# Kernel tuning notes

Hardware: AMD Instinct MI355X
Metric: run time of the kernel (lower is better)

## Reference

```python
import jax, jax.numpy as jnp
import numpy as np

HEADS = 16
DIM_HEAD = 64
LN_EPS = 1e-5
COS_EPS = 1e-8


def setup_inputs() -> dict:
    key = jax.random.key(0)
    ks = jax.random.split(key, 5)
    dim = 1024
    inner = HEADS * DIM_HEAD
    q = jax.random.normal(ks[0], (4, 1024, dim), dtype=jnp.float32)
    k = jax.random.normal(ks[1], (4, 2048, dim), dtype=jnp.float32)
    v = jax.random.normal(ks[2], (4, 2048, dim), dtype=jnp.float32)
    W_in = jax.random.normal(ks[3], (dim, inner), dtype=jnp.float32) * (1.0 / np.sqrt(dim))
    W_out = jax.random.normal(ks[4], (inner, dim), dtype=jnp.float32) * (1.0 / np.sqrt(inner))
    ln_gamma = jnp.ones((dim,), dtype=jnp.float32)
    ln_beta = jnp.zeros((dim,), dtype=jnp.float32)
    b_out = jnp.zeros((dim,), dtype=jnp.float32)
    return {"q": q, "k": k, "v": v, "ln_gamma": ln_gamma, "ln_beta": ln_beta,
            "W_in": W_in, "W_out": W_out, "b_out": b_out}


def _layernorm(x, gamma, beta):
    mu = jnp.mean(x, axis=-1, keepdims=True)
    var = jnp.mean(jnp.square(x - mu), axis=-1, keepdims=True)  # biased, as torch
    return (x - mu) * jax.lax.rsqrt(var + LN_EPS) * gamma + beta


def _project(t, gamma, beta, W_in):
    # LayerNorm -> Linear(no bias) -> split heads: b n (h d) -> b h n d
    x = _layernorm(t, gamma, beta) @ W_in
    b, n, _ = x.shape
    return x.reshape(b, n, HEADS, DIM_HEAD).transpose(0, 2, 1, 3)


def reference(q, k, v, ln_gamma, ln_beta, W_in, W_out, b_out):
    f_q = _project(q, ln_gamma, ln_beta, W_in)  # [b,h,n,d]
    f_k = _project(k, ln_gamma, ln_beta, W_in)  # [b,h,m,d]
    f_v = _project(v, ln_gamma, ln_beta, W_in)  # [b,h,m,d]
    dots = jnp.einsum('bhnd,bhmd->bhnm', f_q, f_k)
    qn = jnp.linalg.norm(f_q, axis=-1, keepdims=True)          # [b,h,n,1]
    kn = jnp.linalg.norm(f_k, axis=-1, keepdims=True)          # [b,h,m,1]
    attn = dots / (qn * kn.transpose(0, 1, 3, 2) + COS_EPS)    # [b,h,n,m]
    out = jnp.einsum('bhnm,bhmd->bhnd', attn, f_v)             # [b,h,n,d]
    b, h, n, d = out.shape
    out = out.transpose(0, 2, 1, 3).reshape(b, n, h * d)       # b n (h d)
    return out @ W_out + b_out
```

## Files before the change

kernel.cpp:

```cpp
#include <hip/hip_runtime.h>

constexpr int BATCH = 4;
constexpr int SEQQ  = 1024;
constexpr int SEQK  = 2048;
constexpr int DIM   = 1024;
constexpr int NH    = 16;
constexpr int DH    = 64;
constexpr int RQ    = BATCH * SEQQ;
constexpr int RK    = BATCH * SEQK;
constexpr int RTOT  = RQ + 2 * RK;
constexpr int BH    = BATCH * NH;
constexpr int NSLC  = 8;
constexpr float LN_EPS = 1e-5f;

typedef _Float16 f16;
typedef __attribute__((ext_vector_type(8))) _Float16 f16x8;
typedef __attribute__((ext_vector_type(4))) float f32x4;

__device__ __forceinline__ void async16(const void* g, void* l) {
  __builtin_amdgcn_global_load_lds(
      (const __attribute__((address_space(1))) void*)g,
      (__attribute__((address_space(3))) void*)l, 16, 0, 0);
}

__global__ void __launch_bounds__(256) ln_to_f16(
    const float* __restrict__ q, const float* __restrict__ k,
    const float* __restrict__ v, const float* __restrict__ gamma,
    const float* __restrict__ beta, f16* __restrict__ a_h) {
  const int row = blockIdx.x * 4 + (threadIdx.x >> 6);
  const int lane = threadIdx.x & 63;
  const float* src;
  if (row < RQ)            src = q + (size_t)row * DIM;
  else if (row < RQ + RK)  src = k + (size_t)(row - RQ) * DIM;
  else                     src = v + (size_t)(row - RQ - RK) * DIM;
  float4 x[4];
  float s = 0.f, s2 = 0.f;
#pragma unroll
  for (int c = 0; c < 4; c++) {
    x[c] = ((const float4*)src)[c * 64 + lane];
    s  += x[c].x + x[c].y + x[c].z + x[c].w;
    s2 += x[c].x * x[c].x + x[c].y * x[c].y + x[c].z * x[c].z + x[c].w * x[c].w;
  }
#pragma unroll
  for (int off = 1; off < 64; off <<= 1) {
    s  += __shfl_xor(s, off);
    s2 += __shfl_xor(s2, off);
  }
  const float mu = s / DIM;
  const float rs = rsqrtf(s2 / DIM - mu * mu + LN_EPS);
#pragma unroll
  for (int c = 0; c < 4; c++) {
    float4 g = ((const float4*)gamma)[c * 64 + lane];
    float4 b = ((const float4*)beta)[c * 64 + lane];
    union { f16 h[4]; uint2 u; } o;
    o.h[0] = (f16)((x[c].x - mu) * rs * g.x + b.x);
    o.h[1] = (f16)((x[c].y - mu) * rs * g.y + b.y);
    o.h[2] = (f16)((x[c].z - mu) * rs * g.z + b.z);
    o.h[3] = (f16)((x[c].w - mu) * rs * g.w + b.w);
    ((uint2*)(a_h + (size_t)row * DIM))[c * 64 + lane] = o.u;
  }
}

__global__ void __launch_bounds__(256) transpose_f16(
    const float* __restrict__ W0, const float* __restrict__ W1,
    f16* __restrict__ T0, f16* __restrict__ T1) {
  const float* W = blockIdx.z ? W1 : W0;
  f16* T = blockIdx.z ? T1 : T0;
  __shared__ float tile[32][33];
  int tx = threadIdx.x & 31, ty = threadIdx.x >> 5;
  int k0 = blockIdx.x * 32, n0 = blockIdx.y * 32;
#pragma unroll
  for (int i = 0; i < 4; i++)
    tile[ty + 8 * i][tx] = W[(size_t)(k0 + ty + 8 * i) * DIM + n0 + tx];
  __syncthreads();
#pragma unroll
  for (int i = 0; i < 4; i++)
    T[(size_t)(n0 + ty + 8 * i) * DIM + k0 + tx] = (f16)tile[tx][ty + 8 * i];
}

template <int MT, bool OUT_F16, bool NORMS, bool BIAS>
__global__ void __launch_bounds__(256) mfma_gemm(
    const f16* __restrict__ A, const f16* __restrict__ Bt,
    void* __restrict__ Cout, const float* __restrict__ bias,
    float* __restrict__ rq, float* __restrict__ rk) {
  constexpr int JT = (MT == 128) ? 4 : 2;
  __shared__ f16 As[2][MT * 32];
  __shared__ f16 Bs[2][128 * 32];
  const int t = threadIdx.x;
  const int wid = t >> 6;
  const int lane = t & 63;
  const int row0 = blockIdx.x * MT;
  const int col0 = blockIdx.y * 128;
  const int wm = (MT == 128) ? (wid >> 1) * 64 : 0;
  const int wn = (MT == 128) ? (wid & 1) * 64 : wid * 32;

  const int rB = 32 * wid + (lane >> 2);
  const int qB = ((lane & 3) - ((rB >> 1) & 3)) & 3;
  const f16* gB = Bt + (size_t)(col0 + rB) * DIM + qB * 8;
  f16* lB0 = Bs[0] + 32 * wid * 32;
  f16* lB1 = Bs[1] + 32 * wid * 32;
  const int rA = (MT == 128 ? 32 : 16) * wid + (lane >> 2);
  const int qA = ((lane & 3) - ((rA >> 1) & 3)) & 3;
  const f16* gA = A + (size_t)(row0 + rA) * DIM + qA * 8;
  f16* lA0 = As[0] + (MT == 128 ? 32 : 16) * wid * 32;
  f16* lA1 = As[1] + (MT == 128 ? 32 : 16) * wid * 32;

  f32x4 acc[4][JT];
#pragma unroll
  for (int i = 0; i < 4; i++)
#pragma unroll
    for (int j = 0; j < JT; j++) acc[i][j] = (f32x4){0.f, 0.f, 0.f, 0.f};

  const int mrow = lane & 15;
  const int kq_p = (((lane >> 4) + ((lane >> 1) & 3)) & 3) * 8;

  for (int kt = 0; kt < DIM / 64; ++kt) {
    if (kt) __syncthreads();
    const int ko = kt * 64;
    async16(gA + ko,      lA0);
    if (MT == 128) async16(gA + ko + 16 * DIM, lA0 + 512);
    async16(gB + ko,      lB0);
    async16(gB + ko + 16 * DIM, lB0 + 512);
    async16(gA + ko + 32, lA1);
    if (MT == 128) async16(gA + ko + 32 + 16 * DIM, lA1 + 512);
    async16(gB + ko + 32, lB1);
    async16(gB + ko + 32 + 16 * DIM, lB1 + 512);
    __syncthreads();

#pragma unroll
    for (int h = 0; h < 2; ++h) {
      f16x8 af[4], bf[JT];
#pragma unroll
      for (int i = 0; i < 4; i++)
        af[i] = *(const f16x8*)(As[h] + (wm + i * 16 + mrow) * 32 + kq_p);
#pragma unroll
      for (int j = 0; j < JT; j++)
        bf[j] = *(const f16x8*)(Bs[h] + (wn + j * 16 + mrow) * 32 + kq_p);
#pragma unroll
      for (int i = 0; i < 4; i++)
#pragma unroll
        for (int j = 0; j < JT; j++)
          acc[i][j] = __builtin_amdgcn_mfma_f32_16x16x32_f16(af[i], bf[j], acc[i][j], 0, 0, 0);
    }
  }

  const int ccol = lane & 15;
  const int crow = (lane >> 4) * 4;
  if (OUT_F16) {
    f16* C = (f16*)Cout;
#pragma unroll
    for (int j = 0; j < JT; j++) {
      const int col = col0 + wn + j * 16 + ccol;
#pragma unroll
      for (int i = 0; i < 4; i++) {
        f16* Cp = C + (size_t)(row0 + wm + i * 16 + crow) * DIM + col;
#pragma unroll
        for (int r = 0; r < 4; r++) Cp[(size_t)r * DIM] = (f16)acc[i][j][r];
      }
    }
  } else {
    float* C = (float*)Cout;
#pragma unroll
    for (int j = 0; j < JT; j++) {
      const int col = col0 + wn + j * 16 + ccol;
      float bv = BIAS ? bias[col] : 0.f;
#pragma unroll
      for (int i = 0; i < 4; i++) {
        float* Cp = C + (size_t)(row0 + wm + i * 16 + crow) * DIM + col;
#pragma unroll
        for (int r = 0; r < 4; r++) Cp[(size_t)r * DIM] = acc[i][j][r] + bv;
      }
    }
  }

  if (NORMS && MT == 128) {
    float sums[4][4];
#pragma unroll
    for (int i = 0; i < 4; i++)
#pragma unroll
      for (int r = 0; r < 4; r++) {
        float s = 0.f;
#pragma unroll
        for (int j = 0; j < JT; j++) s += acc[i][j][r] * acc[i][j][r];
        sums[i][r] = s;
      }
#pragma unroll
    for (int off = 1; off < 16; off <<= 1)
#pragma unroll
      for (int i = 0; i < 4; i++)
#pragma unroll
        for (int r = 0; r < 4; r++)
          sums[i][r] += __shfl_xor(sums[i][r], off);
    if ((lane & 15) == 0) {
      const int head = (col0 + wn) >> 6;
#pragma unroll
      for (int i = 0; i < 4; i++)
#pragma unroll
        for (int r = 0; r < 4; r++) {
          const int row = row0 + wm + i * 16 + crow + r;
          const float inv = rsqrtf(sums[i][r]);
          if (row < RQ)            rq[(size_t)row * NH + head] = inv;
          else if (row < RQ + RK)  rk[(size_t)(row - RQ) * NH + head] = inv;
        }
    }
  }
}

__global__ void __launch_bounds__(256) s_kernel(
    const f16* __restrict__ f, const float* __restrict__ rk,
    float* __restrict__ S4) {
  const int bh = blockIdx.x;
  const int b = bh >> 4, h = bh & 15;
  const int mbase = blockIdx.y * (SEQK / NSLC);
  const int t = threadIdx.x;
  __shared__ float ks[32][68];
  __shared__ float vs[32][68];
  const int lm   = t >> 3;
  const int lseg = (t & 7) * 8;
  const int d1 = (t & 15) * 4;
  const int d2 = (t >> 4) * 4;
  float acc[4][4] = {{0.f}};
  const f16* fk_base = f + ((size_t)RQ + (size_t)b * SEQK) * DIM + h * DH;
  const f16* fv_base = f + ((size_t)RQ + RK + (size_t)b * SEQK) * DIM + h * DH;

  int m = mbase + lm;
  f16x8 kv = *(const f16x8*)(fk_base + (size_t)m * DIM + lseg);
  f16x8 vv = *(const f16x8*)(fv_base + (size_t)m * DIM + lseg);
  float sc = rk[(size_t)(b * SEQK + m) * NH + h];

  constexpr int SUBS = SEQK / NSLC / 32;
  for (int sub = 0; sub < SUBS; ++sub) {
    __syncthreads();
#pragma unroll
    for (int e = 0; e < 8; e++) {
      ks[lm][lseg + e] = (float)kv[e] * sc;
      vs[lm][lseg + e] = (float)vv[e];
    }
    __syncthreads();
    if (sub + 1 < SUBS) {
      m = mbase + (sub + 1) * 32 + lm;
      kv = *(const f16x8*)(fk_base + (size_t)m * DIM + lseg);
      vv = *(const f16x8*)(fv_base + (size_t)m * DIM + lseg);
      sc = rk[(size_t)(b * SEQK + m) * NH + h];
    }
#pragma unroll
    for (int mm = 0; mm < 32; ++mm) {
      float4 kk = *(const float4*)&ks[mm][d1];
      float4 vv2 = *(const float4*)&vs[mm][d2];
      acc[0][0] = fmaf(kk.x, vv2.x, acc[0][0]);
      acc[0][1] = fmaf(kk.x, vv2.y, acc[0][1]);
      acc[0][2] = fmaf(kk.x, vv2.z, acc[0][2]);
      acc[0][3] = fmaf(kk.x, vv2.w, acc[0][3]);
      acc[1][0] = fmaf(kk.y, vv2.x, acc[1][0]);
      acc[1][1] = fmaf(kk.y, vv2.y, acc[1][1]);
      acc[1][2] = fmaf(kk.y, vv2.z, acc[1][2]);
      acc[1][3] = fmaf(kk.y, vv2.w, acc[1][3]);
      acc[2][0] = fmaf(kk.z, vv2.x, acc[2][0]);
      acc[2][1] = fmaf(kk.z, vv2.y, acc[2][1]);
      acc[2][2] = fmaf(kk.z, vv2.z, acc[2][2]);
      acc[2][3] = fmaf(kk.z, vv2.w, acc[2][3]);
      acc[3][0] = fmaf(kk.w, vv2.x, acc[3][0]);
      acc[3][1] = fmaf(kk.w, vv2.y, acc[3][1]);
      acc[3][2] = fmaf(kk.w, vv2.z, acc[3][2]);
      acc[3][3] = fmaf(kk.w, vv2.w, acc[3][3]);
    }
  }
  float* Sp = S4 + ((size_t)blockIdx.y * BH + bh) * DH * DH;
#pragma unroll
  for (int i = 0; i < 4; i++)
#pragma unroll
    for (int j = 0; j < 4; j++)
      Sp[(d1 + i) * DH + (d2 + j)] = acc[i][j];
}

__global__ void __launch_bounds__(256) outhead_kernel(
    const f16* __restrict__ f, const float* __restrict__ S4,
    const float* __restrict__ rq, f16* __restrict__ ao) {
  const int bh = blockIdx.x;
  const int b = bh >> 4, h = bh & 15;
  const int nbase = blockIdx.y * 64;
  const int t = threadIdx.x;
  __shared__ float Sl[64][68];
  __shared__ float Ql[64][68];
  {
    const int r = t >> 2;
    const int seg = (t & 3) * 16;
    const float* Sp = S4 + (size_t)bh * DH * DH + r * DH + seg;
    constexpr size_t STR = (size_t)BH * DH * DH;
#pragma unroll
    for (int c = 0; c < 4; c++) {
      float4 s = {0.f, 0.f, 0.f, 0.f};
#pragma unroll
      for (int p = 0; p < NSLC; p++) {
        float4 sp = ((const float4*)(Sp + p * STR))[c];
        s.x += sp.x; s.y += sp.y; s.z += sp.z; s.w += sp.w;
      }
      *(float4*)&Sl[r][seg + 4 * c] = s;
    }
    const f16* Qp = f + ((size_t)b * SEQQ + nbase + r) * DIM + h * DH + seg;
    f16x8 q0 = *(const f16x8*)Qp;
    f16x8 q1 = *(const f16x8*)(Qp + 8);
#pragma unroll
    for (int e = 0; e < 8; e++) {
      Ql[r][seg + e]     = (float)q0[e];
      Ql[r][seg + 8 + e] = (float)q1[e];
    }
  }
  __syncthreads();
  const int d2 = (t & 15) * 4;
  const int g  = t >> 4;
#pragma unroll
  for (int i = 0; i < 4; ++i) {
    const int n = i * 16 + g;
    float4 acc = {0.f, 0.f, 0.f, 0.f};
#pragma unroll 8
    for (int d1 = 0; d1 < 64; ++d1) {
      float qv = Ql[n][d1];
      float4 sv = *(const float4*)&Sl[d1][d2];
      acc.x = fmaf(qv, sv.x, acc.x);
      acc.y = fmaf(qv, sv.y, acc.y);
      acc.z = fmaf(qv, sv.z, acc.z);
      acc.w = fmaf(qv, sv.w, acc.w);
    }
    const float r = rq[((size_t)b * SEQQ + nbase + n) * NH + h];
    union { f16 h4[4]; uint2 u; } o;
    o.h4[0] = (f16)(acc.x * r);
    o.h4[1] = (f16)(acc.y * r);
    o.h4[2] = (f16)(acc.z * r);
    o.h4[3] = (f16)(acc.w * r);
    *(uint2*)(ao + ((size_t)b * SEQQ + nbase + n) * DIM + h * DH + d2) = o.u;
  }
}

extern "C" void kernel_launch(void* const* d_in, const int* in_sizes, int n_in,
                              void* d_out, int out_size, void* d_ws, size_t ws_size,
                              hipStream_t stream) {
  const float* q     = (const float*)d_in[0];
  const float* k     = (const float*)d_in[1];
  const float* v     = (const float*)d_in[2];
  const float* gamma = (const float*)d_in[3];
  const float* beta  = (const float*)d_in[4];
  const float* W_in  = (const float*)d_in[5];
  const float* W_out = (const float*)d_in[6];
  const float* b_out = (const float*)d_in[7];
  float* out = (float*)d_out;

  char* w = (char*)d_ws;
  f16*   f      = (f16*)w;
  f16*   a_h    = f + (size_t)RTOT * DIM;
  f16*   wt_in  = a_h + (size_t)RTOT * DIM;
  f16*   wt_out = wt_in + (size_t)DIM * DIM;
  float* rqb    = (float*)(wt_out + (size_t)DIM * DIM);
  float* rkb    = rqb + (size_t)RQ * NH;
  float* S4     = rkb + (size_t)RK * NH;
  f16*   ao     = a_h;

  ln_to_f16<<<RTOT / 4, 256, 0, stream>>>(q, k, v, gamma, beta, a_h);
  transpose_f16<<<dim3(DIM / 32, DIM / 32, 2), 256, 0, stream>>>(
      W_in, W_out, wt_in, wt_out);

  mfma_gemm<128, true, true, false><<<dim3(RTOT / 128, DIM / 128), 256, 0, stream>>>(
      a_h, wt_in, f, nullptr, rqb, rkb);

  s_kernel<<<dim3(BH, NSLC), 256, 0, stream>>>(f, rkb, S4);

  outhead_kernel<<<dim3(BH, SEQQ / 64), 256, 0, stream>>>(f, S4, rqb, ao);

  mfma_gemm<64, false, false, true><<<dim3(RQ / 64, DIM / 128), 256, 0, stream>>>(
      ao, wt_out, out, b_out, nullptr, nullptr);
}
```

Before: 244.5 us.

## Fold per-head attention state into per-batch output weight matrix

Row normalisation now happens in the projection GEMM epilogue: each head segment is scaled by its inverse norm before the f16 store, so s_kernel no longer applies key scales. The per-head KᵀV matrices are reduced to f16 and multiplied into W_out to build a per-batch 1024x1024 matrix. The final GEMM then consumes normalized q directly against that matrix, replacing the separate outhead kernel. This trades the q·S pass and ao round-trip for an extra small GEMM, per-batch weight reads, and more f16 rounding of S and M.

```diff
diff --git a/kernel.cpp b/kernel.cpp
--- a/kernel.cpp
+++ b/kernel.cpp
@@ -78,11 +78,10 @@
     T[(size_t)(n0 + ty + 8 * i) * DIM + k0 + tx] = (f16)tile[tx][ty + 8 * i];
 }
 
-template <int MT, bool OUT_F16, bool NORMS, bool BIAS>
+template <int MT, bool OUT_F16, bool NORMS, bool BIAS, bool PERB>
 __global__ void __launch_bounds__(256) mfma_gemm(
     const f16* __restrict__ A, const f16* __restrict__ Bt,
-    void* __restrict__ Cout, const float* __restrict__ bias,
-    float* __restrict__ rq, float* __restrict__ rk) {
+    void* __restrict__ Cout, const float* __restrict__ bias) {
   constexpr int JT = (MT == 128) ? 4 : 2;
   __shared__ f16 As[2][MT * 32];
   __shared__ f16 Bs[2][128 * 32];
@@ -94,9 +93,11 @@
   const int wm = (MT == 128) ? (wid >> 1) * 64 : 0;
   const int wn = (MT == 128) ? (wid & 1) * 64 : wid * 32;
 
+  const f16* BtB = PERB ? Bt + (size_t)(row0 >> 10) * DIM * DIM : Bt;
+
   const int rB = 32 * wid + (lane >> 2);
   const int qB = ((lane & 3) - ((rB >> 1) & 3)) & 3;
-  const f16* gB = Bt + (size_t)(col0 + rB) * DIM + qB * 8;
+  const f16* gB = BtB + (size_t)(col0 + rB) * DIM + qB * 8;
   f16* lB0 = Bs[0] + 32 * wid * 32;
   f16* lB1 = Bs[1] + 32 * wid * 32;
   const int rA = (MT == 128 ? 32 : 16) * wid + (lane >> 2);
@@ -144,6 +145,36 @@
     }
   }
 
+  if (NORMS && MT == 128) {
+    if (row0 < RQ + RK) {
+      float sums[4][4];
+#pragma unroll
+      for (int i = 0; i < 4; i++)
+#pragma unroll
+        for (int r = 0; r < 4; r++) {
+          float s = 0.f;
+#pragma unroll
+          for (int j = 0; j < JT; j++) s += acc[i][j][r] * acc[i][j][r];
+          sums[i][r] = s;
+        }
+#pragma unroll
+      for (int off = 1; off < 16; off <<= 1)
+#pragma unroll
+        for (int i = 0; i < 4; i++)
+#pragma unroll
+          for (int r = 0; r < 4; r++)
+            sums[i][r] += __shfl_xor(sums[i][r], off);
+#pragma unroll
+      for (int i = 0; i < 4; i++)
+#pragma unroll
+        for (int r = 0; r < 4; r++) {
+          const float inv = rsqrtf(sums[i][r]);
+#pragma unroll
+          for (int j = 0; j < JT; j++) acc[i][j][r] *= inv;
+        }
+    }
+  }
+
   const int ccol = lane & 15;
   const int crow = (lane >> 4) * 4;
   if (OUT_F16) {
@@ -172,43 +203,10 @@
       }
     }
   }
-
-  if (NORMS && MT == 128) {
-    float sums[4][4];
-#pragma unroll
-    for (int i = 0; i < 4; i++)
-#pragma unroll
-      for (int r = 0; r < 4; r++) {
-        float s = 0.f;
-#pragma unroll
-        for (int j = 0; j < JT; j++) s += acc[i][j][r] * acc[i][j][r];
-        sums[i][r] = s;
-      }
-#pragma unroll
-    for (int off = 1; off < 16; off <<= 1)
-#pragma unroll
-      for (int i = 0; i < 4; i++)
-#pragma unroll
-        for (int r = 0; r < 4; r++)
-          sums[i][r] += __shfl_xor(sums[i][r], off);
-    if ((lane & 15) == 0) {
-      const int head = (col0 + wn) >> 6;
-#pragma unroll
-      for (int i = 0; i < 4; i++)
-#pragma unroll
-        for (int r = 0; r < 4; r++) {
-          const int row = row0 + wm + i * 16 + crow + r;
-          const float inv = rsqrtf(sums[i][r]);
-          if (row < RQ)            rq[(size_t)row * NH + head] = inv;
-          else if (row < RQ + RK)  rk[(size_t)(row - RQ) * NH + head] = inv;
-        }
-    }
-  }
 }
 
 __global__ void __launch_bounds__(256) s_kernel(
-    const f16* __restrict__ f, const float* __restrict__ rk,
-    float* __restrict__ S4) {
+    const f16* __restrict__ f, float* __restrict__ S4) {
   const int bh = blockIdx.x;
   const int b = bh >> 4, h = bh & 15;
   const int mbase = blockIdx.y * (SEQK / NSLC);
@@ -226,14 +224,13 @@
   int m = mbase + lm;
   f16x8 kv = *(const f16x8*)(fk_base + (size_t)m * DIM + lseg);
   f16x8 vv = *(const f16x8*)(fv_base + (size_t)m * DIM + lseg);
-  float sc = rk[(size_t)(b * SEQK + m) * NH + h];
 
   constexpr int SUBS = SEQK / NSLC / 32;
   for (int sub = 0; sub < SUBS; ++sub) {
     __syncthreads();
 #pragma unroll
     for (int e = 0; e < 8; e++) {
-      ks[lm][lseg + e] = (float)kv[e] * sc;
+      ks[lm][lseg + e] = (float)kv[e];
       vs[lm][lseg + e] = (float)vv[e];
     }
     __syncthreads();
@@ -241,7 +238,6 @@
       m = mbase + (sub + 1) * 32 + lm;
       kv = *(const f16x8*)(fk_base + (size_t)m * DIM + lseg);
       vv = *(const f16x8*)(fv_base + (size_t)m * DIM + lseg);
-      sc = rk[(size_t)(b * SEQK + m) * NH + h];
     }
 #pragma unroll
     for (int mm = 0; mm < 32; ++mm) {
@@ -273,62 +269,87 @@
       Sp[(d1 + i) * DH + (d2 + j)] = acc[i][j];
 }
 
-__global__ void __launch_bounds__(256) outhead_kernel(
-    const f16* __restrict__ f, const float* __restrict__ S4,
-    const float* __restrict__ rq, f16* __restrict__ ao) {
+__global__ void __launch_bounds__(256) s_reduce(
+    const float* __restrict__ S4, f16* __restrict__ Sh) {
   const int bh = blockIdx.x;
+  const int t = threadIdx.x;
+  const size_t base = (size_t)bh * DH * DH + t * 16;
+  constexpr size_t STR = (size_t)BH * DH * DH;
+#pragma unroll
+  for (int c = 0; c < 4; c++) {
+    float4 s = {0.f, 0.f, 0.f, 0.f};
+#pragma unroll
+    for (int p = 0; p < NSLC; p++) {
+      float4 sp = *(const float4*)(S4 + base + p * STR + 4 * c);
+      s.x += sp.x; s.y += sp.y; s.z += sp.z; s.w += sp.w;
+    }
+    union { f16 h[4]; uint2 u; } o;
+    o.h[0] = (f16)s.x; o.h[1] = (f16)s.y; o.h[2] = (f16)s.z; o.h[3] = (f16)s.w;
+    *(uint2*)(Sh + base + 4 * c) = o.u;
+  }
+}
+
+__global__ void __launch_bounds__(256) m_build(
+    const f16* __restrict__ wt_out, const f16* __restrict__ Sh,
+    f16* __restrict__ Mt) {
+  const int n0 = blockIdx.x * 128;
+  const int bh = blockIdx.y;
   const int b = bh >> 4, h = bh & 15;
-  const int nbase = blockIdx.y * 64;
+  __shared__ f16 As[128 * 64];
+  __shared__ f16 Bs[64 * 64];
   const int t = threadIdx.x;
-  __shared__ float Sl[64][68];
-  __shared__ float Ql[64][68];
-  {
-    const int r = t >> 2;
-    const int seg = (t & 3) * 16;
-    const float* Sp = S4 + (size_t)bh * DH * DH + r * DH + seg;
-    constexpr size_t STR = (size_t)BH * DH * DH;
-#pragma unroll
-    for (int c = 0; c < 4; c++) {
-      float4 s = {0.f, 0.f, 0.f, 0.f};
-#pragma unroll
-      for (int p = 0; p < NSLC; p++) {
-        float4 sp = ((const float4*)(Sp + p * STR))[c];
-        s.x += sp.x; s.y += sp.y; s.z += sp.z; s.w += sp.w;
-      }
-      *(float4*)&Sl[r][seg + 4 * c] = s;
-    }
-    const f16* Qp = f + ((size_t)b * SEQQ + nbase + r) * DIM + h * DH + seg;
-    f16x8 q0 = *(const f16x8*)Qp;
-    f16x8 q1 = *(const f16x8*)(Qp + 8);
-#pragma unroll
-    for (int e = 0; e < 8; e++) {
-      Ql[r][seg + e]     = (float)q0[e];
-      Ql[r][seg + 8 + e] = (float)q1[e];
-    }
-  }
+  const int wid = t >> 6, lane = t & 63;
+
+  const f16* gA = wt_out + (size_t)(n0 + 32 * wid + (lane >> 3)) * DIM
+                  + 64 * h + (lane & 7) * 8;
+  f16* lA = As + 32 * wid * 64;
+  const f16* gB = Sh + (size_t)bh * DH * DH + (16 * wid + (lane >> 3)) * 64
+                  + (lane & 7) * 8;
+  f16* lB = Bs + 16 * wid * 64;
+#pragma unroll
+  for (int o = 0; o < 4; o++) async16(gA + (size_t)(8 * o) * DIM, lA + 8 * o * 64);
+  async16(gB, lB);
+  async16(gB + 8 * 64, lB + 8 * 64);
   __syncthreads();
-  const int d2 = (t & 15) * 4;
-  const int g  = t >> 4;
-#pragma unroll
-  for (int i = 0; i < 4; ++i) {
-    const int n = i * 16 + g;
-    float4 acc = {0.f, 0.f, 0.f, 0.f};
-#pragma unroll 8
-    for (int d1 = 0; d1 < 64; ++d1) {
-      float qv = Ql[n][d1];
-      float4 sv = *(const float4*)&Sl[d1][d2];
-      acc.x = fmaf(qv, sv.x, acc.x);
-      acc.y = fmaf(qv, sv.y, acc.y);
-      acc.z = fmaf(qv, sv.z, acc.z);
-      acc.w = fmaf(qv, sv.w, acc.w);
-    }
-    const float r = rq[((size_t)b * SEQQ + nbase + n) * NH + h];
-    union { f16 h4[4]; uint2 u; } o;
-    o.h4[0] = (f16)(acc.x * r);
-    o.h4[1] = (f16)(acc.y * r);
-    o.h4[2] = (f16)(acc.z * r);
-    o.h4[3] = (f16)(acc.w * r);
-    *(uint2*)(ao + ((size_t)b * SEQQ + nbase + n) * DIM + h * DH + d2) = o.u;
+
+  const int wm = (wid >> 1) * 64;
+  const int wn = (wid & 1) * 32;
+  const int mrow = lane & 15;
+  f32x4 acc[4][2];
+#pragma unroll
+  for (int i = 0; i < 4; i++)
+#pragma unroll
+    for (int j = 0; j < 2; j++) acc[i][j] = (f32x4){0.f, 0.f, 0.f, 0.f};
+
+#pragma unroll
+  for (int kh = 0; kh < 2; kh++) {
+    const int kq = kh * 32 + (lane >> 4) * 8;
+    f16x8 af[4], bf[2];
+#pragma unroll
+    for (int i = 0; i < 4; i++)
+      af[i] = *(const f16x8*)(As + (wm + i * 16 + mrow) * 64 + kq);
+#pragma unroll
+    for (int j = 0; j < 2; j++)
+      bf[j] = *(const f16x8*)(Bs + (wn + j * 16 + mrow) * 64 + kq);
+#pragma unroll
+    for (int i = 0; i < 4; i++)
+#pragma unroll
+      for (int j = 0; j < 2; j++)
+        acc[i][j] = __builtin_amdgcn_mfma_f32_16x16x32_f16(af[i], bf[j], acc[i][j], 0, 0, 0);
+  }
+
+  const int ccol = lane & 15;
+  const int crow = (lane >> 4) * 4;
+  f16* Mb = Mt + (size_t)b * DIM * DIM;
+#pragma unroll
+  for (int j = 0; j < 2; j++) {
+    const int col = 64 * h + wn + j * 16 + ccol;
+#pragma unroll
+    for (int i = 0; i < 4; i++) {
+      f16* Mp = Mb + (size_t)(n0 + wm + i * 16 + crow) * DIM + col;
+#pragma unroll
+      for (int r = 0; r < 4; r++) Mp[(size_t)r * DIM] = (f16)acc[i][j][r];
+    }
   }
 }
 
@@ -350,22 +371,23 @@
   f16*   a_h    = f + (size_t)RTOT * DIM;
   f16*   wt_in  = a_h + (size_t)RTOT * DIM;
   f16*   wt_out = wt_in + (size_t)DIM * DIM;
-  float* rqb    = (float*)(wt_out + (size_t)DIM * DIM);
-  float* rkb    = rqb + (size_t)RQ * NH;
-  float* S4     = rkb + (size_t)RK * NH;
-  f16*   ao     = a_h;
+  f16*   Mt     = wt_out + (size_t)DIM * DIM;
+  f16*   Sh     = Mt + (size_t)BATCH * DIM * DIM;
+  float* S4     = (float*)(Sh + (size_t)BH * DH * DH);
 
   ln_to_f16<<<RTOT / 4, 256, 0, stream>>>(q, k, v, gamma, beta, a_h);
   transpose_f16<<<dim3(DIM / 32, DIM / 32, 2), 256, 0, stream>>>(
       W_in, W_out, wt_in, wt_out);
 
-  mfma_gemm<128, true, true, false><<<dim3(RTOT / 128, DIM / 128), 256, 0, stream>>>(
-      a_h, wt_in, f, nullptr, rqb, rkb);
-
-  s_kernel<<<dim3(BH, NSLC), 256, 0, stream>>>(f, rkb, S4);
-
-  outhead_kernel<<<dim3(BH, SEQQ / 64), 256, 0, stream>>>(f, S4, rqb, ao);
-
-  mfma_gemm<64, false, false, true><<<dim3(RQ / 64, DIM / 128), 256, 0, stream>>>(
-      ao, wt_out, out, b_out, nullptr, nullptr);
-}
+  mfma_gemm<128, true, true, false, false>
+      <<<dim3(RTOT / 128, DIM / 128), 256, 0, stream>>>(a_h, wt_in, f, nullptr);
+
+  s_kernel<<<dim3(BH, NSLC), 256, 0, stream>>>(f, S4);
+
+  s_reduce<<<BH, 256, 0, stream>>>(S4, Sh);
+
+  m_build<<<dim3(DIM / 128, BH), 256, 0, stream>>>(wt_out, Sh, Mt);
+
+  mfma_gemm<64, false, false, true, true>
+      <<<dim3(RQ / 64, DIM / 128), 256, 0, stream>>>(f, Mt, out, b_out);
+}
```

Measured after the change: 241.8 us. About the same (-1.1%).
